# Kernel tuning notes

Hardware: AMD Instinct MI355X
Metric: run time of the kernel (lower is better)

Reference implementation:

```python
import jax, jax.numpy as jnp
import numpy as np

MIN_TIMESCALE = 1.0
MAX_TIMESCALE = 10000.0


def llama_rope(x):
    # x: [B, S, N, H]; LLaMA-style interleaved rotary embedding (pairs along last dim).
    B, S, N, H = x.shape
    half = H // 2
    fraction = 2.0 * jnp.arange(0, half, dtype=jnp.float32) / H
    timescale = MIN_TIMESCALE * (MAX_TIMESCALE / MIN_TIMESCALE) ** fraction  # [half]
    position = jnp.arange(S, dtype=jnp.float32)[None, :, None, None]  # [1,S,1,1]
    sinusoid = position / timescale[None, None, None, :]  # [1,S,1,half]
    sin, cos = jnp.sin(sinusoid), jnp.cos(sinusoid)
    xr = x.astype(jnp.float32).reshape(B, S, N, half, 2)
    x1, x2 = xr[..., 0], xr[..., 1]
    r1 = x1 * cos - x2 * sin
    r2 = x2 * cos + x1 * sin
    out = jnp.stack((r1, r2), axis=-1).reshape(B, S, N, H)
    return out.astype(x.dtype)


def setup_inputs() -> dict:
    key = jax.random.key(0)
    kx, kq, kk, kv, ko = jax.random.split(key, 5)
    B, S, D, N, H = 4, 2048, 2048, 16, 128
    x = jax.random.normal(kx, (B, S, D), dtype=jnp.float32)
    # fan_in-style scaling for projection kernels
    wq = jax.random.normal(kq, (D, N, H), dtype=jnp.float32) / np.sqrt(D)
    wk = jax.random.normal(kk, (D, N, H), dtype=jnp.float32) / np.sqrt(D)
    wv = jax.random.normal(kv, (D, N, H), dtype=jnp.float32) / np.sqrt(D)
    wo = jax.random.normal(ko, (N, H, D), dtype=jnp.float32) / np.sqrt(N * H)
    return {"x": x, "wq": wq, "wk": wk, "wv": wv, "wo": wo}


def reference(x, wq, wk, wv, wo):
    # QKV projections (DenseGeneral with features=(num_heads, head_dim))
    q = jnp.einsum("bsd,dnh->bsnh", x, wq)
    k = jnp.einsum("bsd,dnh->bsnh", x, wk)
    v = jnp.einsum("bsd,dnh->bsnh", x, wv)
    # Fused RoPE on query and key (LLaMA interleaved variant)
    q = llama_rope(q)
    k = llama_rope(k)
    head_dim = q.shape[-1]
    q = q / jnp.sqrt(jnp.asarray(head_dim, q.dtype))
    # Causal flash attention (math equivalent: masked softmax attention)
    S = q.shape[1]
    logits = jnp.einsum("bqnh,bknh->bnqk", q, k)  # [B,N,S,S]
    causal = jnp.tril(jnp.ones((S, S), dtype=bool))
    logits = jnp.where(causal[None, None, :, :], logits, jnp.asarray(-1e30, logits.dtype))
    probs = jax.nn.softmax(logits.astype(jnp.float32), axis=-1).astype(v.dtype)
    attn = jnp.einsum("bnqk,bknh->bqnh", probs, v)  # [B,S,N,H]
    # Output projection (DenseGeneral over axes (-2,-1))
    return jnp.einsum("bqnh,nhd->bqd", attn, wo)
```

## Files before the change

kernel.cpp:

```cpp
#include <hip/hip_runtime.h>
#include <hip/hip_bf16.h>
#include <cmath>

#define S_LEN 2048
#define DDIM  2048
#define NHEAD 16
#define HDIM  128
#define BATCH 4
#define KPAD  152
#define VPAD  40
#define PPAD  40

typedef __bf16 bf16;
typedef __attribute__((ext_vector_type(8))) __bf16 bf16x8;
typedef __attribute__((ext_vector_type(4))) __bf16 bf16x4;
typedef __attribute__((ext_vector_type(4))) float  f32x4;

__device__ __forceinline__ void gl_lds(const bf16* g, bf16* l) {
  __builtin_amdgcn_global_load_lds((const __attribute__((address_space(1))) unsigned*)g,
                                   (__attribute__((address_space(3))) unsigned*)l, 16, 0, 0);
}

__global__ __launch_bounds__(256)
void conv_kernel(const float* __restrict__ x, bf16* __restrict__ y) {
  size_t i = ((size_t)blockIdx.x * 256 + threadIdx.x) * 8;
  float4 a = *(const float4*)&x[i];
  float4 b = *(const float4*)&x[i + 4];
  bf16x8 o;
  o[0] = (bf16)a.x; o[1] = (bf16)a.y; o[2] = (bf16)a.z; o[3] = (bf16)a.w;
  o[4] = (bf16)b.x; o[5] = (bf16)b.y; o[6] = (bf16)b.z; o[7] = (bf16)b.w;
  *(bf16x8*)&y[i] = o;
}

__global__ __launch_bounds__(256)
void twconv_kernel(const float* __restrict__ W, bf16* __restrict__ Wt) {
  __shared__ bf16 tile[64][72];
  const int t  = threadIdx.x;
  const int k0 = blockIdx.x * 64;
  const int n0 = blockIdx.y * 64;
#pragma unroll
  for (int it = 0; it < 4; it++) {
    int k = (t >> 4) + it * 16;
    int n = (t & 15) * 4;
    float4 v = *(const float4*)&W[(size_t)(k0 + k) * DDIM + n0 + n];
    tile[k][n + 0] = (bf16)v.x; tile[k][n + 1] = (bf16)v.y;
    tile[k][n + 2] = (bf16)v.z; tile[k][n + 3] = (bf16)v.w;
  }
  __syncthreads();
#pragma unroll
  for (int it = 0; it < 2; it++) {
    int n  = (t >> 3) + it * 32;
    int kc = (t & 7) * 8;
    bf16x8 o;
#pragma unroll
    for (int j = 0; j < 8; j++) o[j] = tile[kc + j][n];
    *(bf16x8*)&Wt[(size_t)(n0 + n) * DDIM + k0 + kc] = o;
  }
}

template <int MODE>
__global__ __launch_bounds__(512, 2)
void gemm_kernel(const bf16* __restrict__ A, const bf16* __restrict__ Bt,
                 void* __restrict__ Out) {
  __shared__ bf16 As[2][256 * 64];
  __shared__ bf16 Bs[2][256 * 64];

  const int t    = threadIdx.x;
  const int m0   = blockIdx.y * 256;
  const int n0   = blockIdx.x * 256;
  const int lane = t & 63;
  const int wave = t >> 6;
  const int wm   = wave >> 2;
  const int wn   = wave & 3;
  const int quad = lane >> 4;
  const int lm   = lane & 15;
  const int sw   = lm & 7;

  const int lrow   = lane >> 3;
  const int lslot  = lane & 7;
  const int lchunk = lslot ^ lrow;

  const int rA = wm * 128 + wn * 32;
  const int rB = (wn >> 1) * 128 + (wm * 2 + (wn & 1)) * 32;
  const bf16* gA = &A [(size_t)(m0 + rA + lrow) * DDIM + lchunk * 8];
  const bf16* gB = &Bt[(size_t)(n0 + rB + lrow) * DDIM + lchunk * 8];

  f32x4 acc[8][4];
#pragma unroll
  for (int i = 0; i < 8; i++)
#pragma unroll
    for (int j = 0; j < 4; j++) acc[i][j] = (f32x4){0.f, 0.f, 0.f, 0.f};

  auto stage = [&](int k0, int b) {
#pragma unroll
    for (int q = 0; q < 4; q++) {
      gl_lds(gA + (size_t)q * 8 * DDIM + k0, &As[b][(rA + q * 8) * 64]);
      gl_lds(gB + (size_t)q * 8 * DDIM + k0, &Bs[b][(rB + q * 8) * 64]);
    }
  };

  stage(0, 0);
  stage(64, 1);
  asm volatile("s_waitcnt vmcnt(8)" ::: "memory");
  __builtin_amdgcn_s_barrier();

  const int NT = DDIM / 64;
#pragma unroll 2
  for (int tt = 0; tt < NT; ++tt) {
    const bf16* as = &As[tt & 1][0];
    const bf16* bs = &Bs[tt & 1][0];
    bf16x8 af[4], bfr[4];

#pragma unroll
    for (int j = 0; j < 4; j++)
      bfr[j] = *(const bf16x8*)&bs[(wn * 64 + j * 16 + lm) * 64 + 8 * (quad ^ sw)];
#pragma unroll
    for (int i = 0; i < 4; i++)
      af[i] = *(const bf16x8*)&as[(wm * 128 + i * 16 + lm) * 64 + 8 * (quad ^ sw)];
    __builtin_amdgcn_s_setprio(1);
#pragma unroll
    for (int i = 0; i < 4; i++)
#pragma unroll
      for (int j = 0; j < 4; j++)
        acc[i][j] = __builtin_amdgcn_mfma_f32_16x16x32_bf16(af[i], bfr[j], acc[i][j], 0, 0, 0);
    __builtin_amdgcn_s_setprio(0);
    __builtin_amdgcn_sched_barrier(0);

#pragma unroll
    for (int i = 0; i < 4; i++)
      af[i] = *(const bf16x8*)&as[(wm * 128 + 64 + i * 16 + lm) * 64 + 8 * (quad ^ sw)];
    __builtin_amdgcn_s_setprio(1);
#pragma unroll
    for (int i = 0; i < 4; i++)
#pragma unroll
      for (int j = 0; j < 4; j++)
        acc[4 + i][j] = __builtin_amdgcn_mfma_f32_16x16x32_bf16(af[i], bfr[j], acc[4 + i][j], 0, 0, 0);
    __builtin_amdgcn_s_setprio(0);
    __builtin_amdgcn_sched_barrier(0);

#pragma unroll
    for (int j = 0; j < 4; j++)
      bfr[j] = *(const bf16x8*)&bs[(wn * 64 + j * 16 + lm) * 64 + 8 * ((4 + quad) ^ sw)];
#pragma unroll
    for (int i = 0; i < 4; i++)
      af[i] = *(const bf16x8*)&as[(wm * 128 + i * 16 + lm) * 64 + 8 * ((4 + quad) ^ sw)];
    __builtin_amdgcn_s_setprio(1);
#pragma unroll
    for (int i = 0; i < 4; i++)
#pragma unroll
      for (int j = 0; j < 4; j++)
        acc[i][j] = __builtin_amdgcn_mfma_f32_16x16x32_bf16(af[i], bfr[j], acc[i][j], 0, 0, 0);
    __builtin_amdgcn_s_setprio(0);
    __builtin_amdgcn_sched_barrier(0);

#pragma unroll
    for (int i = 0; i < 4; i++)
      af[i] = *(const bf16x8*)&as[(wm * 128 + 64 + i * 16 + lm) * 64 + 8 * ((4 + quad) ^ sw)];
    __builtin_amdgcn_s_setprio(1);
#pragma unroll
    for (int i = 0; i < 4; i++)
#pragma unroll
      for (int j = 0; j < 4; j++)
        acc[4 + i][j] = __builtin_amdgcn_mfma_f32_16x16x32_bf16(af[i], bfr[j], acc[4 + i][j], 0, 0, 0);
    __builtin_amdgcn_s_setprio(0);
    __builtin_amdgcn_sched_barrier(0);

    asm volatile("s_waitcnt lgkmcnt(0)" ::: "memory");
    __builtin_amdgcn_s_barrier();
    if (tt + 2 < NT) {
      stage((tt + 2) * 64, tt & 1);
      asm volatile("s_waitcnt vmcnt(8)" ::: "memory");
      __builtin_amdgcn_s_barrier();
    } else if (tt + 1 < NT) {
      asm volatile("s_waitcnt vmcnt(0)" ::: "memory");
      __builtin_amdgcn_s_barrier();
    }
  }

  const int row_base = m0 + wm * 128;
  const int col_base = n0 + wn * 64;

  if constexpr (MODE == 3) {
    float* O = (float*)Out;
#pragma unroll
    for (int m = 0; m < 8; m++)
#pragma unroll
      for (int j = 0; j < 4; j++)
#pragma unroll
        for (int r = 0; r < 4; r++) {
          int row = row_base + (m >> 2) * 64 + (m & 3) * 16 + quad * 4 + r;
          int col = col_base + j * 16 + lm;
          O[(size_t)row * DDIM + col] = acc[m][j][r];
        }
  } else if constexpr (MODE == 2) {
    bf16* O = (bf16*)Out;
#pragma unroll
    for (int m = 0; m < 8; m++) {
      int row = row_base + (m >> 2) * 64 + (m & 3) * 16 + quad * 4;
      int b = row >> 11, s = row & (S_LEN - 1);
#pragma unroll
      for (int j = 0; j < 4; j++) {
        int col = col_base + j * 16 + lm;
        int head = col >> 7, h = col & (HDIM - 1);
        bf16x4 pk;
#pragma unroll
        for (int r = 0; r < 4; r++) pk[r] = (bf16)acc[m][j][r];
        *(bf16x4*)&O[((size_t)(b * NHEAD + head) * HDIM + h) * S_LEN + s] = pk;
      }
    }
  } else {
    bf16* O = (bf16*)Out;
#pragma unroll
    for (int m = 0; m < 8; m++)
#pragma unroll
      for (int j = 0; j < 4; j++)
#pragma unroll
        for (int r = 0; r < 4; r++) {
          int row = row_base + (m >> 2) * 64 + (m & 3) * 16 + quad * 4 + r;
          int col = col_base + j * 16 + lm;
          int b = row >> 11, s = row & (S_LEN - 1);
          int head = col >> 7, h = col & (HDIM - 1);
          float v = acc[m][j][r];
          float partner = __shfl_xor(v, 1, 64);
          float inv_ts = __expf((float)(h >> 1) * -0.14391156831f);
          float ang = (float)s * inv_ts;
          float sn, cs;
          __sincosf(ang, &sn, &cs);
          float o = ((h & 1) == 0) ? (v * cs - partner * sn) : (v * cs + partner * sn);
          if (MODE == 0) o *= 0.08838834764831845f;
          O[((size_t)(b * NHEAD + head) * S_LEN + s) * HDIM + h] = (bf16)o;
        }
  }
}

__global__ __launch_bounds__(512, 2)
void attn_kernel(const bf16* __restrict__ Q, const bf16* __restrict__ K,
                 const bf16* __restrict__ Vt, bf16* __restrict__ Aout) {
  __shared__ bf16 Ks[32 * KPAD];
  __shared__ bf16 Vs[128 * VPAD];
  __shared__ bf16 Pl[8][32 * PPAD];
  const int t    = threadIdx.x;
  const int lane = t & 63;
  const int wave = t >> 6;
  const int quad = lane >> 4;
  const int lm   = lane & 15;
  const int lin  = blockIdx.y * 8 + blockIdx.x;
  const int xcd  = lin & 7;
  const int j    = lin >> 3;
  const int bh   = xcd * 8 + (j >> 3);
  const int ja   = j & 7;
  const int a    = (ja & 1) ? (7 - (ja >> 1)) : (ja >> 1);
  const int lobase = a * 128 + wave * 16;
  const int hibase = 2048 - a * 128 - 128 + wave * 16;
  const size_t hb = (size_t)bh * S_LEN * HDIM;
  const bf16* Qh = Q + hb;
  const bf16* Kh = K + hb;
  const bf16* Vh = Vt + hb;
  bf16* P = &Pl[wave][0];

  bf16x8 qflo[4], qfhi[4];
#pragma unroll
  for (int c = 0; c < 4; c++) {
    qflo[c] = *(const bf16x8*)&Qh[(size_t)(lobase + lm) * HDIM + c * 32 + quad * 8];
    qfhi[c] = *(const bf16x8*)&Qh[(size_t)(hibase + lm) * HDIM + c * 32 + quad * 8];
  }

  bf16 onev = (bf16)1.0f;
  bf16x8 ones = {onev, onev, onev, onev, onev, onev, onev, onev};

  f32x4 olo[8], ohi[8];
#pragma unroll
  for (int hc = 0; hc < 8; hc++) {
    olo[hc] = (f32x4){0.f, 0.f, 0.f, 0.f};
    ohi[hc] = (f32x4){0.f, 0.f, 0.f, 0.f};
  }
  f32x4 llo = (f32x4){0.f, 0.f, 0.f, 0.f};
  f32x4 lhi = (f32x4){0.f, 0.f, 0.f, 0.f};

  const int nkt = 64 - 4 * a;
  const int nlo = 4 * a + (wave >> 1) + 1;
  const int nhi = 61 - 4 * a + (wave >> 1);

  const int krow0 = t >> 4, kcol0 = (t & 15) * 8;
  const int vrow0 = t >> 2, vcol0 = (t & 3) * 8;

  for (int kt = 0; kt < nkt; kt++) {
    const int kb = kt * 32;
    __syncthreads();
    {
      const bf16* kg = &Kh[(size_t)(kb + krow0) * HDIM + kcol0];
      *(bf16x8*)&Ks[krow0 * KPAD + kcol0] = *(const bf16x8*)kg;
      const bf16* vg = &Vh[(size_t)vrow0 * S_LEN + kb + vcol0];
      *(bf16x8*)&Vs[vrow0 * VPAD + vcol0] = *(const bf16x8*)vg;
    }
    __syncthreads();

    const bool hi_act = kt < nhi;
    const bool lo_act = kt < nlo;

    bf16x8 af[2][4];
#pragma unroll
    for (int cb = 0; cb < 2; cb++)
#pragma unroll
      for (int c = 0; c < 4; c++)
        af[cb][c] = *(const bf16x8*)&Ks[(cb * 16 + lm) * KPAD + c * 32 + quad * 8];

    if (hi_act) {
      f32x4 s[2] = {(f32x4){0.f, 0.f, 0.f, 0.f}, (f32x4){0.f, 0.f, 0.f, 0.f}};
#pragma unroll
      for (int c = 0; c < 4; c++)
#pragma unroll
        for (int cb = 0; cb < 2; cb++)
          s[cb] = __builtin_amdgcn_mfma_f32_16x16x32_bf16(af[cb][c], qfhi[c], s[cb], 0, 0, 0);
#pragma unroll
      for (int cb = 0; cb < 2; cb++) {
        bf16x4 pk;
#pragma unroll
        for (int r = 0; r < 4; r++) {
          int key = kb + cb * 16 + quad * 4 + r;
          float sv = (key <= hibase + lm) ? s[cb][r] : -3.0e38f;
          pk[r] = (bf16)__expf(sv - 12.0f);
        }
        *(bf16x4*)&P[(16 + lm) * PPAD + cb * 16 + quad * 4] = pk;
      }
    }
    if (lo_act) {
      f32x4 s[2] = {(f32x4){0.f, 0.f, 0.f, 0.f}, (f32x4){0.f, 0.f, 0.f, 0.f}};
#pragma unroll
      for (int c = 0; c < 4; c++)
#pragma unroll
        for (int cb = 0; cb < 2; cb++)
          s[cb] = __builtin_amdgcn_mfma_f32_16x16x32_bf16(af[cb][c], qflo[c], s[cb], 0, 0, 0);
#pragma unroll
      for (int cb = 0; cb < 2; cb++) {
        bf16x4 pk;
#pragma unroll
        for (int r = 0; r < 4; r++) {
          int key = kb + cb * 16 + quad * 4 + r;
          float sv = (key <= lobase + lm) ? s[cb][r] : -3.0e38f;
          pk[r] = (bf16)__expf(sv - 12.0f);
        }
        *(bf16x4*)&P[lm * PPAD + cb * 16 + quad * 4] = pk;
      }
    }
    __builtin_amdgcn_s_waitcnt(0xC07F);

    bf16x8 vf[8];
#pragma unroll
    for (int hc = 0; hc < 8; hc++)
      vf[hc] = *(const bf16x8*)&Vs[(hc * 16 + lm) * VPAD + quad * 8];

    if (hi_act) {
      bf16x8 pf = *(const bf16x8*)&P[(16 + lm) * PPAD + quad * 8];
#pragma unroll
      for (int hc = 0; hc < 8; hc++)
        ohi[hc] = __builtin_amdgcn_mfma_f32_16x16x32_bf16(pf, vf[hc], ohi[hc], 0, 0, 0);
      lhi = __builtin_amdgcn_mfma_f32_16x16x32_bf16(pf, ones, lhi, 0, 0, 0);
    }
    if (lo_act) {
      bf16x8 pf = *(const bf16x8*)&P[lm * PPAD + quad * 8];
#pragma unroll
      for (int hc = 0; hc < 8; hc++)
        olo[hc] = __builtin_amdgcn_mfma_f32_16x16x32_bf16(pf, vf[hc], olo[hc], 0, 0, 0);
      llo = __builtin_amdgcn_mfma_f32_16x16x32_bf16(pf, ones, llo, 0, 0, 0);
    }
  }

  const int b = bh >> 4, n = bh & 15;
#pragma unroll
  for (int r = 0; r < 4; r++) {
    float invl = 1.0f / llo[r];
    float invh = 1.0f / lhi[r];
    int ql = lobase + quad * 4 + r;
    int qh = hibase + quad * 4 + r;
    size_t bl = ((size_t)(b * S_LEN + ql) * NHEAD + n) * HDIM;
    size_t bhh = ((size_t)(b * S_LEN + qh) * NHEAD + n) * HDIM;
#pragma unroll
    for (int hc = 0; hc < 8; hc++) {
      Aout[bl  + hc * 16 + lm] = (bf16)(olo[hc][r] * invl);
      Aout[bhh + hc * 16 + lm] = (bf16)(ohi[hc][r] * invh);
    }
  }
}

extern "C" void kernel_launch(void* const* d_in, const int* in_sizes, int n_in,
                              void* d_out, int out_size, void* d_ws, size_t ws_size,
                              hipStream_t stream) {
  const float* x  = (const float*)d_in[0];
  const float* wq = (const float*)d_in[1];
  const float* wk = (const float*)d_in[2];
  const float* wv = (const float*)d_in[3];
  const float* wo = (const float*)d_in[4];
  float* out = (float*)d_out;

  const size_t SZ  = (size_t)BATCH * S_LEN * NHEAD * HDIM;
  const size_t WSZ = (size_t)DDIM * DDIM;
  bf16* Qb = (bf16*)d_ws;
  bf16* Kb = Qb + SZ;
  bf16* Vb = Kb + SZ;
  bf16* Eb = Vb + SZ;

  bf16* WTq = (bf16*)d_out;
  bf16* WTk = WTq + WSZ;
  bf16* WTv = WTk + WSZ;
  bf16* WTo = (bf16*)Qb;

  dim3 blk(256);
  conv_kernel<<<SZ / (256 * 8), blk, 0, stream>>>(x, Eb);
  dim3 gt(32, 32);
  twconv_kernel<<<gt, blk, 0, stream>>>(wq, WTq);
  twconv_kernel<<<gt, blk, 0, stream>>>(wk, WTk);
  twconv_kernel<<<gt, blk, 0, stream>>>(wv, WTv);

  dim3 blk2(512);
  dim3 gg(DDIM / 256, (BATCH * S_LEN) / 256);
  gemm_kernel<0><<<gg, blk2, 0, stream>>>(Eb, WTq, (void*)Qb);
  gemm_kernel<1><<<gg, blk2, 0, stream>>>(Eb, WTk, (void*)Kb);
  gemm_kernel<2><<<gg, blk2, 0, stream>>>(Eb, WTv, (void*)Vb);

  dim3 ga(8, BATCH * NHEAD);
  attn_kernel<<<ga, blk2, 0, stream>>>(Qb, Kb, Vb, Eb);

  twconv_kernel<<<gt, blk, 0, stream>>>(wo, WTo);
  gemm_kernel<3><<<gg, blk2, 0, stream>>>(Eb, WTo, (void*)out);
}
```

Baseline: 598.8 us.

## Double-buffer K/V tiles with register prefetch and one barrier per iteration

The attention loop now keeps two LDS buffers for K and V. Each tile is loaded from global memory two iterations ahead into registers and written to LDS one iteration ahead, which cuts the loop to a single __syncthreads per iteration. This is meant to hide global-load latency behind the MFMA work. The QK^T MFMAs for the hi and lo query blocks are issued back to back before the exp step, and the V fragment reads are moved earlier to overlap them. In exchange it uses more LDS and registers, which could lower occupancy under launch_bounds(512,2).

```diff
diff --git a/kernel.cpp b/kernel.cpp
--- a/kernel.cpp
+++ b/kernel.cpp
@@ -236,8 +236,8 @@
 __global__ __launch_bounds__(512, 2)
 void attn_kernel(const bf16* __restrict__ Q, const bf16* __restrict__ K,
                  const bf16* __restrict__ Vt, bf16* __restrict__ Aout) {
-  __shared__ bf16 Ks[32 * KPAD];
-  __shared__ bf16 Vs[128 * VPAD];
+  __shared__ bf16 Ks[2][32 * KPAD];
+  __shared__ bf16 Vs[2][128 * VPAD];
   __shared__ bf16 Pl[8][32 * PPAD];
   const int t    = threadIdx.x;
   const int lane = t & 63;
@@ -284,16 +284,28 @@
   const int krow0 = t >> 4, kcol0 = (t & 15) * 8;
   const int vrow0 = t >> 2, vcol0 = (t & 3) * 8;
 
+  bf16x8 kr, vr;
+
+  auto ldk = [&](int kt) {
+    kr = *(const bf16x8*)&Kh[(size_t)(kt * 32 + krow0) * HDIM + kcol0];
+    vr = *(const bf16x8*)&Vh[(size_t)vrow0 * S_LEN + kt * 32 + vcol0];
+  };
+  auto stw = [&](int b) {
+    *(bf16x8*)&Ks[b][krow0 * KPAD + kcol0] = kr;
+    *(bf16x8*)&Vs[b][vrow0 * VPAD + vcol0] = vr;
+  };
+
+  ldk(0);
+  stw(0);
+  if (nkt > 1) ldk(1);
+  __syncthreads();
+
   for (int kt = 0; kt < nkt; kt++) {
-    const int kb = kt * 32;
-    __syncthreads();
-    {
-      const bf16* kg = &Kh[(size_t)(kb + krow0) * HDIM + kcol0];
-      *(bf16x8*)&Ks[krow0 * KPAD + kcol0] = *(const bf16x8*)kg;
-      const bf16* vg = &Vh[(size_t)vrow0 * S_LEN + kb + vcol0];
-      *(bf16x8*)&Vs[vrow0 * VPAD + vcol0] = *(const bf16x8*)vg;
-    }
-    __syncthreads();
+    const int kb  = kt * 32;
+    const int cur = kt & 1;
+
+    if (kt + 1 < nkt) stw((kt + 1) & 1);
+    if (kt + 2 < nkt) ldk(kt + 2);
 
     const bool hi_act = kt < nhi;
     const bool lo_act = kt < nlo;
@@ -303,41 +315,51 @@
     for (int cb = 0; cb < 2; cb++)
 #pragma unroll
       for (int c = 0; c < 4; c++)
-        af[cb][c] = *(const bf16x8*)&Ks[(cb * 16 + lm) * KPAD + c * 32 + quad * 8];
-
+        af[cb][c] = *(const bf16x8*)&Ks[cur][(cb * 16 + lm) * KPAD + c * 32 + quad * 8];
+
+    f32x4 shi[2] = {(f32x4){0.f, 0.f, 0.f, 0.f}, (f32x4){0.f, 0.f, 0.f, 0.f}};
+    f32x4 slo[2] = {(f32x4){0.f, 0.f, 0.f, 0.f}, (f32x4){0.f, 0.f, 0.f, 0.f}};
     if (hi_act) {
-      f32x4 s[2] = {(f32x4){0.f, 0.f, 0.f, 0.f}, (f32x4){0.f, 0.f, 0.f, 0.f}};
 #pragma unroll
       for (int c = 0; c < 4; c++)
 #pragma unroll
         for (int cb = 0; cb < 2; cb++)
-          s[cb] = __builtin_amdgcn_mfma_f32_16x16x32_bf16(af[cb][c], qfhi[c], s[cb], 0, 0, 0);
+          shi[cb] = __builtin_amdgcn_mfma_f32_16x16x32_bf16(af[cb][c], qfhi[c], shi[cb], 0, 0, 0);
+    }
+    if (lo_act) {
+#pragma unroll
+      for (int c = 0; c < 4; c++)
+#pragma unroll
+        for (int cb = 0; cb < 2; cb++)
+          slo[cb] = __builtin_amdgcn_mfma_f32_16x16x32_bf16(af[cb][c], qflo[c], slo[cb], 0, 0, 0);
+    }
+
+    bf16x8 vf[8];
+#pragma unroll
+    for (int hc = 0; hc < 8; hc++)
+      vf[hc] = *(const bf16x8*)&Vs[cur][(hc * 16 + lm) * VPAD + quad * 8];
+
+    if (hi_act) {
 #pragma unroll
       for (int cb = 0; cb < 2; cb++) {
         bf16x4 pk;
 #pragma unroll
         for (int r = 0; r < 4; r++) {
           int key = kb + cb * 16 + quad * 4 + r;
-          float sv = (key <= hibase + lm) ? s[cb][r] : -3.0e38f;
+          float sv = (key <= hibase + lm) ? shi[cb][r] : -3.0e38f;
           pk[r] = (bf16)__expf(sv - 12.0f);
         }
         *(bf16x4*)&P[(16 + lm) * PPAD + cb * 16 + quad * 4] = pk;
       }
     }
     if (lo_act) {
-      f32x4 s[2] = {(f32x4){0.f, 0.f, 0.f, 0.f}, (f32x4){0.f, 0.f, 0.f, 0.f}};
-#pragma unroll
-      for (int c = 0; c < 4; c++)
-#pragma unroll
-        for (int cb = 0; cb < 2; cb++)
-          s[cb] = __builtin_amdgcn_mfma_f32_16x16x32_bf16(af[cb][c], qflo[c], s[cb], 0, 0, 0);
 #pragma unroll
       for (int cb = 0; cb < 2; cb++) {
         bf16x4 pk;
 #pragma unroll
         for (int r = 0; r < 4; r++) {
           int key = kb + cb * 16 + quad * 4 + r;
-          float sv = (key <= lobase + lm) ? s[cb][r] : -3.0e38f;
+          float sv = (key <= lobase + lm) ? slo[cb][r] : -3.0e38f;
           pk[r] = (bf16)__expf(sv - 12.0f);
         }
         *(bf16x4*)&P[lm * PPAD + cb * 16 + quad * 4] = pk;
@@ -345,11 +367,6 @@
     }
     __builtin_amdgcn_s_waitcnt(0xC07F);
 
-    bf16x8 vf[8];
-#pragma unroll
-    for (int hc = 0; hc < 8; hc++)
-      vf[hc] = *(const bf16x8*)&Vs[(hc * 16 + lm) * VPAD + quad * 8];
-
     if (hi_act) {
       bf16x8 pf = *(const bf16x8*)&P[(16 + lm) * PPAD + quad * 8];
 #pragma unroll
@@ -364,6 +381,7 @@
         olo[hc] = __builtin_amdgcn_mfma_f32_16x16x32_bf16(pf, vf[hc], olo[hc], 0, 0, 0);
       llo = __builtin_amdgcn_mfma_f32_16x16x32_bf16(pf, ones, llo, 0, 0, 0);
     }
+    __syncthreads();
   }
 
   const int b = bh >> 4, n = bh & 15;
```

Result: faster. 574.9 us (-4.0%).
